# Kernel optimization log

Measured on AMD Instinct MI355X. Metric: run time of the kernel, lower is better.

Reference implementation:

```python
import jax, jax.numpy as jnp
import numpy as np

# dims: H hops, N nodes, F = nfeat, HID = hidden, C = nclass
H, N, F, HID, C = 10, 100000, 256, 512, 47
ALPHA = 0.5  # GCNII alpha in FeedForwardNetII


def setup_inputs() -> dict:
    key = jax.random.key(0)
    ks = jax.random.split(key, 16)
    s = lambda i, shape, scale: jax.random.normal(ks[i], shape, jnp.float32) * scale
    return {
        "features": s(0, (H, N, F), 1.0),        # stacked feature_list
        "label_emb": s(1, (N, C), 1.0),
        # lr_att: Linear(2F, 1)
        "wa": s(2, (2 * F,), 0.05),
        "ba": jnp.zeros((), jnp.float32),
        # lr_output = FeedForwardNetII(F, HID, C, n_layers_2=4, alpha)
        "w0": s(3, (F, HID), 0.05), "b0": jnp.zeros((HID,), jnp.float32),
        "wg1": s(4, (HID, HID), 0.04),
        "wg2": s(5, (HID, HID), 0.04),
        "w_last": s(6, (HID, C), 0.05), "b_last": jnp.zeros((C,), jnp.float32),
        "a_out": jnp.full((), 0.25, jnp.float32),  # PReLU slope
        # label_fc = FeedForwardNet(C, HID, C, n_layers_3=4)
        "wl0": s(7, (C, HID), 0.1), "bl0": jnp.zeros((HID,), jnp.float32),
        "wl1": s(8, (HID, HID), 0.04), "bl1": jnp.zeros((HID,), jnp.float32),
        "wl2": s(9, (HID, HID), 0.04), "bl2": jnp.zeros((HID,), jnp.float32),
        "wl3": s(10, (HID, C), 0.05), "bl3": jnp.zeros((C,), jnp.float32),
        "a_lab": jnp.full((), 0.25, jnp.float32),
    }


def _prelu(x, a):
    return jnp.where(x >= 0, x, a * x)


def _act(x):  # act = leaky_relu(0.2)
    return jax.nn.leaky_relu(x, 0.2)


def reference(features, label_emb, wa, ba, w0, b0, wg1, wg2, w_last, b_last, a_out,
              wl0, bl0, wl1, bl1, wl2, bl2, wl3, bl3, a_lab):
    # lr_att(cat([a, b])) == a @ wl + b @ wr + ba
    wl, wr = wa[:F], wa[F:]
    xr = jnp.einsum('hnf,f->hn', features, wr)  # right-half projection of each hop
    # hop 0: cat([X0, X0])
    scores = [_act(features[0] @ wl + xr[0] + ba)]  # list of [N]
    for i in range(1, H):
        att = jax.nn.softmax(jnp.stack(scores, axis=1), axis=1)       # [N, i]
        history = jnp.einsum('hnf,nh->nf', features[:i], att)          # [N, F]
        scores.append(_act(history @ wl + xr[i] + ba))
    att = jax.nn.softmax(jnp.stack(scores, axis=1), axis=1)            # [N, H]
    right = jnp.einsum('hnf,nh->nf', features, att)                    # [N, F]

    x = right @ w0 + b0
    h0 = x
    for wg in (wg1, wg2):
        xi = _prelu(x, a_out)
        support = (1.0 - ALPHA) * xi + ALPHA * h0
        x = support @ wg + xi  # GraphConvolution adds its input back
    x = _prelu(x, a_out) @ w_last + b_last                             # [N, C]

    # label_fc: FeedForwardNet, 4 linear layers with PReLU between
    y = _prelu(label_emb @ wl0 + bl0, a_lab)
    y = _prelu(y @ wl1 + bl1, a_lab)
    y = _prelu(y @ wl2 + bl2, a_lab)
    y = y @ wl3 + bl3                                                  # [N, C]
    return x + y
```

## Files before the change

### kernel.cpp

```cpp
#include <hip/hip_runtime.h>
#include <cstdint>
#include <cstddef>


#define DEVI __device__ __forceinline__

typedef __attribute__((ext_vector_type(4))) float fx4;
typedef __attribute__((ext_vector_type(8))) short sx8;

constexpr int NN = 100000;

DEVI unsigned short f2b(float f) {
  unsigned u = __float_as_uint(f);
  u = (u + 0x7fffu + ((u >> 16) & 1u)) >> 16;
  return (unsigned short)u;
}
DEVI float b2f(short v) {
  return __uint_as_float(((unsigned)(unsigned short)v) << 16);
}

#define GLDS16(gp, lp) __builtin_amdgcn_global_load_lds( \
    (__attribute__((address_space(1))) void*)(void*)(gp), \
    (__attribute__((address_space(3))) void*)(lp), 16, 0, 0)

__global__ __launch_bounds__(256)
void attn_kernel(const float* __restrict__ feat, const float* __restrict__ wa,
                 const float* __restrict__ baP, short* __restrict__ right) {
  const int lane = threadIdx.x & 63;
  const int n = blockIdx.x * 4 + (threadIdx.x >> 6);
  const float ba = *baP;
  const fx4 wl4 = *(const fx4*)(wa + lane * 4);
  const fx4 wr4 = *(const fx4*)(wa + 256 + lane * 4);
  fx4 f[10];
  float xl[10], xr[10];
#pragma unroll
  for (int h = 0; h < 10; h++) {
    f[h] = *(const fx4*)(feat + ((long)h * NN + n) * 256 + lane * 4);
    float pl = f[h][0] * wl4[0] + f[h][1] * wl4[1] + f[h][2] * wl4[2] + f[h][3] * wl4[3];
    float pr = f[h][0] * wr4[0] + f[h][1] * wr4[1] + f[h][2] * wr4[2] + f[h][3] * wr4[3];
#pragma unroll
    for (int off = 32; off > 0; off >>= 1) {
      pl += __shfl_xor(pl, off);
      pr += __shfl_xor(pr, off);
    }
    xl[h] = pl; xr[h] = pr;
  }
  float e[10];
  float s = xl[0] + xr[0] + ba;
  s = s >= 0.f ? s : 0.2f * s;
  e[0] = __expf(s);
  float P = e[0] * xl[0], S = e[0];
#pragma unroll
  for (int i = 1; i < 10; i++) {
    float t = P / S + xr[i] + ba;
    t = t >= 0.f ? t : 0.2f * t;
    e[i] = __expf(t);
    P += e[i] * xl[i];
    S += e[i];
  }
  const float inv = 1.f / S;
  fx4 r = {0.f, 0.f, 0.f, 0.f};
#pragma unroll
  for (int h = 0; h < 10; h++) {
    const float w = e[h] * inv;
    r[0] += w * f[h][0]; r[1] += w * f[h][1];
    r[2] += w * f[h][2]; r[3] += w * f[h][3];
  }
  ushort4 o;
  o.x = f2b(r[0]); o.y = f2b(r[1]); o.z = f2b(r[2]); o.w = f2b(r[3]);
  *(ushort4*)(right + (long)n * 256 + lane * 4) = o;
}

__global__ void pack_wt(const float* __restrict__ src, short* __restrict__ dst,
                        int Ksrc, int Nsrc, int padK, int padN) {
  int idx = blockIdx.x * 256 + threadIdx.x;
  if (idx >= padK * padN) return;
  int n = idx / padK, k = idx - n * padK;
  float v = (k < Ksrc && n < Nsrc) ? src[(long)k * Nsrc + n] : 0.f;
  dst[idx] = (short)f2b(v);
}

__global__ void pack_lab(const float* __restrict__ src, short* __restrict__ dst) {
  long idx = (long)blockIdx.x * 256 + threadIdx.x;
  if (idx >= (long)NN * 64) return;
  int n = (int)(idx >> 6), k = (int)(idx & 63);
  dst[idx] = (short)f2b(k < 47 ? src[(long)n * 47 + k] : 0.f);
}

template<int BN, int EPI>
__global__ __launch_bounds__(256)
void gemm_bt(const short* __restrict__ A, const short* __restrict__ BT, const int K,
             const float* __restrict__ bias, const short* __restrict__ epiIn,
             short* __restrict__ out0, short* __restrict__ out1,
             const float* __restrict__ alphaP, const float* __restrict__ xout,
             float* __restrict__ fout) {
  constexpr int BM = 128, BK = 32;
  constexpr int WN = BN / 2;
  constexpr int FM = 4, FN = WN / 16;
  __shared__ short As[BM * BK];
  __shared__ short Bs[BN * BK];
  const int tid = threadIdx.x;
  const int wave = tid >> 6, lane = tid & 63;
  const int wm = wave >> 1, wn = wave & 1;
  const int m0 = blockIdx.x * BM;
  const int n0 = blockIdx.y * BN;
  fx4 acc[FM][FN] = {};

  const int kIters = K / BK;
  for (int kk = 0; kk < kIters; kk++) {
    const int k0 = kk * BK;
#pragma unroll
    for (int c = 0; c < (BM * BK) / (256 * 8); c++) {
      const int idx = c * 256 + tid;
      long row = m0 + (idx >> 2);
      if (row > NN - 1) row = NN - 1;
      const short* gp = A + row * (long)K + k0 + ((idx & 3) << 3);
      GLDS16(gp, As + idx * 8);
    }
#pragma unroll
    for (int c = 0; c < (BN * BK) / (256 * 8); c++) {
      const int idx = c * 256 + tid;
      const short* gp = BT + (long)(n0 + (idx >> 2)) * K + k0 + ((idx & 3) << 3);
      GLDS16(gp, Bs + idx * 8);
    }
    __syncthreads();
    sx8 af[FM], bf[FN];
#pragma unroll
    for (int i = 0; i < FM; i++)
      af[i] = *(const sx8*)(As + (wm * 64 + i * 16 + (lane & 15)) * BK + ((lane >> 4) << 3));
#pragma unroll
    for (int j = 0; j < FN; j++)
      bf[j] = *(const sx8*)(Bs + (wn * WN + j * 16 + (lane & 15)) * BK + ((lane >> 4) << 3));
#pragma unroll
    for (int i = 0; i < FM; i++)
#pragma unroll
      for (int j = 0; j < FN; j++)
        acc[i][j] = __builtin_amdgcn_mfma_f32_16x16x32_bf16(af[i], bf[j], acc[i][j], 0, 0, 0);
    __syncthreads();
  }

  const float alpha = (alphaP != nullptr) ? *alphaP : 0.f;
#pragma unroll
  for (int i = 0; i < FM; i++) {
#pragma unroll
    for (int j = 0; j < FN; j++) {
#pragma unroll
      for (int r = 0; r < 4; r++) {
        const int m = m0 + wm * 64 + i * 16 + ((lane >> 4) << 2) + r;
        const int n = n0 + wn * WN + j * 16 + (lane & 15);
        if (m >= NN) continue;
        float v = acc[i][j][r];
        const long o = (long)m * 512 + n;
        if constexpr (EPI == 0) {
          v += bias[n];
          out0[o] = (short)f2b(v);
          const float p = v >= 0.f ? v : alpha * v;
          out1[o] = (short)f2b(0.5f * p + 0.5f * v);
        } else if constexpr (EPI == 1) {
          const float x0v = b2f(epiIn[o]);
          const float xi = x0v >= 0.f ? x0v : alpha * x0v;
          const float x1 = v + xi;
          out0[o] = (short)f2b(x1);
          const float p1 = x1 >= 0.f ? x1 : alpha * x1;
          out1[o] = (short)f2b(0.5f * p1 + 0.5f * x0v);
        } else if constexpr (EPI == 2) {
          const float x1v = b2f(epiIn[o]);
          const float xi = x1v >= 0.f ? x1v : alpha * x1v;
          const float x2 = v + xi;
          out0[o] = (short)f2b(x2 >= 0.f ? x2 : alpha * x2);
        } else if constexpr (EPI == 3) {
          const float bv = (n < 47) ? bias[n] : 0.f;
          fout[(long)m * 64 + n] = v + bv;
        } else if constexpr (EPI == 4) {
          const float y = v + bias[n];
          out0[o] = (short)f2b(y >= 0.f ? y : alpha * y);
        } else {
          if (n < 47) fout[(long)m * 47 + n] = v + bias[n] + xout[(long)m * 64 + n];
        }
      }
    }
  }
}

constexpr long  OFF_W0T  = 0;
constexpr long  OFF_WG1T = 131072;
constexpr long  OFF_WG2T = 393216;
constexpr long  OFF_WLST = 655360;
constexpr long  OFF_WL0T = 688128;
constexpr long  OFF_WL1T = 720896;
constexpr long  OFF_WL2T = 983040;
constexpr long  OFF_WL3T = 1245184;
constexpr size_t B_RIGHT = 2560000;
constexpr size_t B_LAB   = 53760000;
constexpr size_t B_XOUT  = 66560000;
constexpr size_t B_B1    = 92160000;
constexpr size_t B_B2    = 194560000;
constexpr size_t B_B3    = 296960000;
constexpr size_t B_B4    = 399360000;
constexpr size_t WS_NEED = 501760000;

extern "C" void kernel_launch(void* const* d_in, const int* in_sizes, int n_in,
                              void* d_out, int out_size, void* d_ws, size_t ws_size,
                              hipStream_t stream) {
  const float* features  = (const float*)d_in[0];
  const float* label_emb = (const float*)d_in[1];
  const float* wa     = (const float*)d_in[2];
  const float* ba     = (const float*)d_in[3];
  const float* w0     = (const float*)d_in[4];
  const float* b0     = (const float*)d_in[5];
  const float* wg1    = (const float*)d_in[6];
  const float* wg2    = (const float*)d_in[7];
  const float* w_last = (const float*)d_in[8];
  const float* b_last = (const float*)d_in[9];
  const float* a_out  = (const float*)d_in[10];
  const float* wl0    = (const float*)d_in[11];
  const float* bl0    = (const float*)d_in[12];
  const float* wl1    = (const float*)d_in[13];
  const float* bl1    = (const float*)d_in[14];
  const float* wl2    = (const float*)d_in[15];
  const float* bl2    = (const float*)d_in[16];
  const float* wl3    = (const float*)d_in[17];
  const float* bl3    = (const float*)d_in[18];
  const float* a_lab  = (const float*)d_in[19];

  if (ws_size < WS_NEED) return;

  char*  ws    = (char*)d_ws;
  short* WP    = (short*)ws;
  short* right = (short*)(ws + B_RIGHT);
  short* lab   = (short*)(ws + B_LAB);
  float* xoutb = (float*)(ws + B_XOUT);
  short* B1    = (short*)(ws + B_B1);
  short* B2    = (short*)(ws + B_B2);
  short* B3    = (short*)(ws + B_B3);
  short* B4    = (short*)(ws + B_B4);

  auto pk = [&](const float* s, long off, int Ks, int Ns, int pK, int pN) {
    int tot = pK * pN;
    pack_wt<<<dim3((tot + 255) / 256), dim3(256), 0, stream>>>(s, WP + off, Ks, Ns, pK, pN);
  };
  pk(w0,     OFF_W0T,  256, 512, 256, 512);
  pk(wg1,    OFF_WG1T, 512, 512, 512, 512);
  pk(wg2,    OFF_WG2T, 512, 512, 512, 512);
  pk(w_last, OFF_WLST, 512, 47,  512, 64);
  pk(wl0,    OFF_WL0T, 47,  512, 64,  512);
  pk(wl1,    OFF_WL1T, 512, 512, 512, 512);
  pk(wl2,    OFF_WL2T, 512, 512, 512, 512);
  pk(wl3,    OFF_WL3T, 512, 47,  512, 64);
  pack_lab<<<dim3(25000), dim3(256), 0, stream>>>(label_emb, lab);

  attn_kernel<<<dim3(25000), dim3(256), 0, stream>>>(features, wa, ba, right);

  const dim3 blk(256);
  const dim3 g512(782, 4), g64(782, 1);
  gemm_bt<128, 0><<<g512, blk, 0, stream>>>(right, WP + OFF_W0T, 256, b0, nullptr,
                                            B1, B2, a_out, nullptr, nullptr);
  gemm_bt<128, 1><<<g512, blk, 0, stream>>>(B2, WP + OFF_WG1T, 512, nullptr, B1,
                                            B3, B4, a_out, nullptr, nullptr);
  gemm_bt<128, 2><<<g512, blk, 0, stream>>>(B4, WP + OFF_WG2T, 512, nullptr, B3,
                                            B1, nullptr, a_out, nullptr, nullptr);
  gemm_bt<64, 3><<<g64, blk, 0, stream>>>(B1, WP + OFF_WLST, 512, b_last, nullptr,
                                          nullptr, nullptr, nullptr, nullptr, xoutb);
  gemm_bt<128, 4><<<g512, blk, 0, stream>>>(lab, WP + OFF_WL0T, 64, bl0, nullptr,
                                            B2, nullptr, a_lab, nullptr, nullptr);
  gemm_bt<128, 4><<<g512, blk, 0, stream>>>(B2, WP + OFF_WL1T, 512, bl1, nullptr,
                                            B3, nullptr, a_lab, nullptr, nullptr);
  gemm_bt<128, 4><<<g512, blk, 0, stream>>>(B3, WP + OFF_WL2T, 512, bl2, nullptr,
                                            B4, nullptr, a_lab, nullptr, nullptr);
  gemm_bt<64, 5><<<g64, blk, 0, stream>>>(B4, WP + OFF_WL3T, 512, bl3, nullptr,
                                          nullptr, nullptr, nullptr, xoutb, (float*)d_out);
}
```

Measured before the change: 2.350 ms.

## Pair branch GEMMs per launch, fuse final projections, merge packing kernels

Replaces the nine packing kernels with a single packing kernel. The GCNII branch and the label_fc branch now run side by side, one layer of each per dual-GEMM launch, so each launch fills more of the GPU. The two output projections (w_last and wl3) are concatenated along K into one GEMM that writes the final sum directly. This removes the fp32 xout intermediate and several launches, at the cost of a larger workspace; when the workspace is too small, a sequential fallback path is used.

```diff
diff --git a/kernel.cpp b/kernel.cpp
--- a/kernel.cpp
+++ b/kernel.cpp
@@ -71,133 +71,222 @@
   *(ushort4*)(right + (long)n * 256 + lane * 4) = o;
 }
 
-__global__ void pack_wt(const float* __restrict__ src, short* __restrict__ dst,
-                        int Ksrc, int Nsrc, int padK, int padN) {
-  int idx = blockIdx.x * 256 + threadIdx.x;
-  if (idx >= padK * padN) return;
-  int n = idx / padK, k = idx - n * padK;
-  float v = (k < Ksrc && n < Nsrc) ? src[(long)k * Nsrc + n] : 0.f;
-  dst[idx] = (short)f2b(v);
-}
-
-__global__ void pack_lab(const float* __restrict__ src, short* __restrict__ dst) {
-  long idx = (long)blockIdx.x * 256 + threadIdx.x;
-  if (idx >= (long)NN * 64) return;
-  int n = (int)(idx >> 6), k = (int)(idx & 63);
-  dst[idx] = (short)f2b(k < 47 ? src[(long)n * 47 + k] : 0.f);
-}
-
-template<int BN, int EPI>
+constexpr int W_W0  = 0;
+constexpr int W_WG1 = 131072;
+constexpr int W_WG2 = 393216;
+constexpr int W_WL0 = 655360;
+constexpr int W_WL1 = 688128;
+constexpr int W_WL2 = 950272;
+constexpr int W_FIN = 1212416;
+constexpr int W_END = 1277952;
+
 __global__ __launch_bounds__(256)
-void gemm_bt(const short* __restrict__ A, const short* __restrict__ BT, const int K,
-             const float* __restrict__ bias, const short* __restrict__ epiIn,
-             short* __restrict__ out0, short* __restrict__ out1,
-             const float* __restrict__ alphaP, const float* __restrict__ xout,
-             float* __restrict__ fout) {
-  constexpr int BM = 128, BK = 32;
-  constexpr int WN = BN / 2;
-  constexpr int FM = 4, FN = WN / 16;
+void uber_pack(const float* __restrict__ w0,     const float* __restrict__ wg1,
+               const float* __restrict__ wg2,    const float* __restrict__ wl0,
+               const float* __restrict__ wl1,    const float* __restrict__ wl2,
+               const float* __restrict__ w_last, const float* __restrict__ wl3,
+               const float* __restrict__ lemb,
+               short* __restrict__ WP, short* __restrict__ lab) {
+  const long idx = (long)blockIdx.x * 256 + threadIdx.x;
+  constexpr long LAB_END = (long)W_END + (long)NN * 64;
+  if (idx >= LAB_END) return;
+  if (idx < W_WG1) {
+    int l = (int)idx, n = l >> 8, k = l & 255;
+    WP[idx] = (short)f2b(w0[(long)k * 512 + n]);
+  } else if (idx < W_WG2) {
+    int l = (int)(idx - W_WG1), n = l >> 9, k = l & 511;
+    WP[idx] = (short)f2b(wg1[(long)k * 512 + n]);
+  } else if (idx < W_WL0) {
+    int l = (int)(idx - W_WG2), n = l >> 9, k = l & 511;
+    WP[idx] = (short)f2b(wg2[(long)k * 512 + n]);
+  } else if (idx < W_WL1) {
+    int l = (int)(idx - W_WL0), n = l >> 6, k = l & 63;
+    WP[idx] = (short)f2b(k < 47 ? wl0[(long)k * 512 + n] : 0.f);
+  } else if (idx < W_WL2) {
+    int l = (int)(idx - W_WL1), n = l >> 9, k = l & 511;
+    WP[idx] = (short)f2b(wl1[(long)k * 512 + n]);
+  } else if (idx < W_FIN) {
+    int l = (int)(idx - W_WL2), n = l >> 9, k = l & 511;
+    WP[idx] = (short)f2b(wl2[(long)k * 512 + n]);
+  } else if (idx < W_FIN + 32768) {
+    int l = (int)(idx - W_FIN), n = l >> 9, k = l & 511;
+    WP[W_FIN + (long)n * 1024 + k] = (short)f2b(n < 47 ? w_last[(long)k * 47 + n] : 0.f);
+  } else if (idx < W_END) {
+    int l = (int)(idx - (W_FIN + 32768)), n = l >> 9, k = l & 511;
+    WP[W_FIN + (long)n * 1024 + 512 + k] = (short)f2b(n < 47 ? wl3[(long)k * 47 + n] : 0.f);
+  } else {
+    long l = idx - W_END;
+    int n = (int)(l >> 6), k = (int)(l & 63);
+    lab[l] = (short)f2b(k < 47 ? lemb[(long)n * 47 + k] : 0.f);
+  }
+}
+
+struct GArgs {
+  const short* A; const short* BT; int K;
+  const float* bias; const short* epiIn;
+  short* out0; short* out1; const float* alphaP;
+};
+
+template<int EPI>
+DEVI void epilogue(const GArgs& g, const fx4 (&acc)[4][4],
+                   int m0, int n0, int wm, int wn, int lane) {
+  const float alpha = (g.alphaP != nullptr) ? *g.alphaP : 0.f;
+#pragma unroll
+  for (int i = 0; i < 4; i++) {
+#pragma unroll
+    for (int j = 0; j < 4; j++) {
+#pragma unroll
+      for (int r = 0; r < 4; r++) {
+        const int m = m0 + wm * 64 + i * 16 + ((lane >> 4) << 2) + r;
+        const int n = n0 + wn * 64 + j * 16 + (lane & 15);
+        if (m >= NN) continue;
+        float v = acc[i][j][r];
+        const long o = (long)m * 512 + n;
+        if constexpr (EPI == 0) {
+          v += g.bias[n];
+          g.out0[o] = (short)f2b(v);
+          const float p = v >= 0.f ? v : alpha * v;
+          g.out1[o] = (short)f2b(0.5f * p + 0.5f * v);
+        } else if constexpr (EPI == 1) {
+          const float x0v = b2f(g.epiIn[o]);
+          const float xi = x0v >= 0.f ? x0v : alpha * x0v;
+          const float x1 = v + xi;
+          g.out0[o] = (short)f2b(x1);
+          const float p1 = x1 >= 0.f ? x1 : alpha * x1;
+          g.out1[o] = (short)f2b(0.5f * p1 + 0.5f * x0v);
+        } else if constexpr (EPI == 2) {
+          const float x1v = b2f(g.epiIn[o]);
+          const float xi = x1v >= 0.f ? x1v : alpha * x1v;
+          const float x2 = v + xi;
+          g.out0[o] = (short)f2b(x2 >= 0.f ? x2 : alpha * x2);
+        } else {
+          const float y = v + g.bias[n];
+          g.out0[o] = (short)f2b(y >= 0.f ? y : alpha * y);
+        }
+      }
+    }
+  }
+}
+
+template<int EA, int EB>
+__global__ __launch_bounds__(256)
+void gemm_dual(GArgs ga, GArgs gb) {
+  constexpr int BM = 128, BN = 128, BK = 32;
+  __shared__ short As[BM * BK];
+  __shared__ short Bs[BN * BK];
+  const bool second = (blockIdx.y >= 4);
+  const short* __restrict__ A  = second ? gb.A  : ga.A;
+  const short* __restrict__ BT = second ? gb.BT : ga.BT;
+  const int K = second ? gb.K : ga.K;
+  const int tid = threadIdx.x;
+  const int wave = tid >> 6, lane = tid & 63;
+  const int wm = wave >> 1, wn = wave & 1;
+  const int m0 = blockIdx.x * BM;
+  const int n0 = (blockIdx.y & 3) * BN;
+  fx4 acc[4][4] = {};
+
+  const int kIters = K / BK;
+  for (int kk = 0; kk < kIters; kk++) {
+    const int k0 = kk * BK;
+#pragma unroll
+    for (int c = 0; c < 2; c++) {
+      const int idx = c * 256 + tid;
+      long row = m0 + (idx >> 2);
+      if (row > NN - 1) row = NN - 1;
+      GLDS16(A + row * (long)K + k0 + ((idx & 3) << 3), As + idx * 8);
+    }
+#pragma unroll
+    for (int c = 0; c < 2; c++) {
+      const int idx = c * 256 + tid;
+      GLDS16(BT + (long)(n0 + (idx >> 2)) * K + k0 + ((idx & 3) << 3), Bs + idx * 8);
+    }
+    __syncthreads();
+    sx8 af[4], bf[4];
+#pragma unroll
+    for (int i = 0; i < 4; i++)
+      af[i] = *(const sx8*)(As + (wm * 64 + i * 16 + (lane & 15)) * BK + ((lane >> 4) << 3));
+#pragma unroll
+    for (int j = 0; j < 4; j++)
+      bf[j] = *(const sx8*)(Bs + (wn * 64 + j * 16 + (lane & 15)) * BK + ((lane >> 4) << 3));
+#pragma unroll
+    for (int i = 0; i < 4; i++)
+#pragma unroll
+      for (int j = 0; j < 4; j++)
+        acc[i][j] = __builtin_amdgcn_mfma_f32_16x16x32_bf16(af[i], bf[j], acc[i][j], 0, 0, 0);
+    __syncthreads();
+  }
+
+  if (!second) epilogue<EA>(ga, acc, m0, n0, wm, wn, lane);
+  else         epilogue<EB>(gb, acc, m0, n0, wm, wn, lane);
+}
+
+__global__ __launch_bounds__(256)
+void gemm_final(const short* __restrict__ Ap, const short* __restrict__ Ay,
+                const short* __restrict__ BT, const float* __restrict__ b1,
+                const float* __restrict__ b2, float* __restrict__ outp) {
+  constexpr int BM = 128, BN = 64, BK = 32, WN = 32;
   __shared__ short As[BM * BK];
   __shared__ short Bs[BN * BK];
   const int tid = threadIdx.x;
   const int wave = tid >> 6, lane = tid & 63;
   const int wm = wave >> 1, wn = wave & 1;
   const int m0 = blockIdx.x * BM;
-  const int n0 = blockIdx.y * BN;
-  fx4 acc[FM][FN] = {};
-
-  const int kIters = K / BK;
-  for (int kk = 0; kk < kIters; kk++) {
+  fx4 acc[4][2] = {};
+
+  for (int kk = 0; kk < 32; kk++) {
     const int k0 = kk * BK;
-#pragma unroll
-    for (int c = 0; c < (BM * BK) / (256 * 8); c++) {
+    const short* __restrict__ Asel = (kk < 16) ? Ap : Ay;
+    const int kl = k0 & 511;
+#pragma unroll
+    for (int c = 0; c < 2; c++) {
       const int idx = c * 256 + tid;
       long row = m0 + (idx >> 2);
       if (row > NN - 1) row = NN - 1;
-      const short* gp = A + row * (long)K + k0 + ((idx & 3) << 3);
-      GLDS16(gp, As + idx * 8);
-    }
-#pragma unroll
-    for (int c = 0; c < (BN * BK) / (256 * 8); c++) {
-      const int idx = c * 256 + tid;
-      const short* gp = BT + (long)(n0 + (idx >> 2)) * K + k0 + ((idx & 3) << 3);
-      GLDS16(gp, Bs + idx * 8);
+      GLDS16(Asel + row * 512L + kl + ((idx & 3) << 3), As + idx * 8);
+    }
+    {
+      const int idx = tid;
+      GLDS16(BT + (long)(idx >> 2) * 1024 + k0 + ((idx & 3) << 3), Bs + idx * 8);
     }
     __syncthreads();
-    sx8 af[FM], bf[FN];
-#pragma unroll
-    for (int i = 0; i < FM; i++)
+    sx8 af[4], bf[2];
+#pragma unroll
+    for (int i = 0; i < 4; i++)
       af[i] = *(const sx8*)(As + (wm * 64 + i * 16 + (lane & 15)) * BK + ((lane >> 4) << 3));
 #pragma unroll
-    for (int j = 0; j < FN; j++)
+    for (int j = 0; j < 2; j++)
       bf[j] = *(const sx8*)(Bs + (wn * WN + j * 16 + (lane & 15)) * BK + ((lane >> 4) << 3));
 #pragma unroll
-    for (int i = 0; i < FM; i++)
-#pragma unroll
-      for (int j = 0; j < FN; j++)
+    for (int i = 0; i < 4; i++)
+#pragma unroll
+      for (int j = 0; j < 2; j++)
         acc[i][j] = __builtin_amdgcn_mfma_f32_16x16x32_bf16(af[i], bf[j], acc[i][j], 0, 0, 0);
     __syncthreads();
   }
 
-  const float alpha = (alphaP != nullptr) ? *alphaP : 0.f;
-#pragma unroll
-  for (int i = 0; i < FM; i++) {
-#pragma unroll
-    for (int j = 0; j < FN; j++) {
+#pragma unroll
+  for (int i = 0; i < 4; i++)
+#pragma unroll
+    for (int j = 0; j < 2; j++)
 #pragma unroll
       for (int r = 0; r < 4; r++) {
         const int m = m0 + wm * 64 + i * 16 + ((lane >> 4) << 2) + r;
-        const int n = n0 + wn * WN + j * 16 + (lane & 15);
-        if (m >= NN) continue;
-        float v = acc[i][j][r];
-        const long o = (long)m * 512 + n;
-        if constexpr (EPI == 0) {
-          v += bias[n];
-          out0[o] = (short)f2b(v);
-          const float p = v >= 0.f ? v : alpha * v;
-          out1[o] = (short)f2b(0.5f * p + 0.5f * v);
-        } else if constexpr (EPI == 1) {
-          const float x0v = b2f(epiIn[o]);
-          const float xi = x0v >= 0.f ? x0v : alpha * x0v;
-          const float x1 = v + xi;
-          out0[o] = (short)f2b(x1);
-          const float p1 = x1 >= 0.f ? x1 : alpha * x1;
-          out1[o] = (short)f2b(0.5f * p1 + 0.5f * x0v);
-        } else if constexpr (EPI == 2) {
-          const float x1v = b2f(epiIn[o]);
-          const float xi = x1v >= 0.f ? x1v : alpha * x1v;
-          const float x2 = v + xi;
-          out0[o] = (short)f2b(x2 >= 0.f ? x2 : alpha * x2);
-        } else if constexpr (EPI == 3) {
-          const float bv = (n < 47) ? bias[n] : 0.f;
-          fout[(long)m * 64 + n] = v + bv;
-        } else if constexpr (EPI == 4) {
-          const float y = v + bias[n];
-          out0[o] = (short)f2b(y >= 0.f ? y : alpha * y);
-        } else {
-          if (n < 47) fout[(long)m * 47 + n] = v + bias[n] + xout[(long)m * 64 + n];
-        }
+        const int n = wn * WN + j * 16 + (lane & 15);
+        if (m < NN && n < 47)
+          outp[(long)m * 47 + n] = acc[i][j][r] + b1[n] + b2[n];
       }
-    }
-  }
-}
-
-constexpr long  OFF_W0T  = 0;
-constexpr long  OFF_WG1T = 131072;
-constexpr long  OFF_WG2T = 393216;
-constexpr long  OFF_WLST = 655360;
-constexpr long  OFF_WL0T = 688128;
-constexpr long  OFF_WL1T = 720896;
-constexpr long  OFF_WL2T = 983040;
-constexpr long  OFF_WL3T = 1245184;
+}
+
 constexpr size_t B_RIGHT = 2560000;
 constexpr size_t B_LAB   = 53760000;
-constexpr size_t B_XOUT  = 66560000;
-constexpr size_t B_B1    = 92160000;
-constexpr size_t B_B2    = 194560000;
-constexpr size_t B_B3    = 296960000;
-constexpr size_t B_B4    = 399360000;
-constexpr size_t WS_NEED = 501760000;
+constexpr size_t B_B1    = 66560000;
+constexpr size_t B_B2    = 168960000;
+constexpr size_t B_B3    = 271360000;
+constexpr size_t B_B4    = 373760000;
+constexpr size_t B_B5    = 476160000;
+constexpr size_t B_B6    = 578560000;
+constexpr size_t WS_PRIMARY  = 680960000;
+constexpr size_t WS_FALLBACK = 476160000;
 
 extern "C" void kernel_launch(void* const* d_in, const int* in_sizes, int n_in,
                               void* d_out, int out_size, void* d_ws, size_t ws_size,
@@ -223,50 +312,53 @@
   const float* bl3    = (const float*)d_in[18];
   const float* a_lab  = (const float*)d_in[19];
 
-  if (ws_size < WS_NEED) return;
+  if (ws_size < WS_FALLBACK) return;
 
   char*  ws    = (char*)d_ws;
   short* WP    = (short*)ws;
   short* right = (short*)(ws + B_RIGHT);
   short* lab   = (short*)(ws + B_LAB);
-  float* xoutb = (float*)(ws + B_XOUT);
-  short* B1    = (short*)(ws + B_B1);
-  short* B2    = (short*)(ws + B_B2);
-  short* B3    = (short*)(ws + B_B3);
-  short* B4    = (short*)(ws + B_B4);
-
-  auto pk = [&](const float* s, long off, int Ks, int Ns, int pK, int pN) {
-    int tot = pK * pN;
-    pack_wt<<<dim3((tot + 255) / 256), dim3(256), 0, stream>>>(s, WP + off, Ks, Ns, pK, pN);
-  };
-  pk(w0,     OFF_W0T,  256, 512, 256, 512);
-  pk(wg1,    OFF_WG1T, 512, 512, 512, 512);
-  pk(wg2,    OFF_WG2T, 512, 512, 512, 512);
-  pk(w_last, OFF_WLST, 512, 47,  512, 64);
-  pk(wl0,    OFF_WL0T, 47,  512, 64,  512);
-  pk(wl1,    OFF_WL1T, 512, 512, 512, 512);
-  pk(wl2,    OFF_WL2T, 512, 512, 512, 512);
-  pk(wl3,    OFF_WL3T, 512, 47,  512, 64);
-  pack_lab<<<dim3(25000), dim3(256), 0, stream>>>(label_emb, lab);
+  short* C1    = (short*)(ws + B_B1);
+  short* C2    = (short*)(ws + B_B2);
+  short* C3    = (short*)(ws + B_B3);
+  short* C4    = (short*)(ws + B_B4);
+
+  uber_pack<<<dim3(29992), dim3(256), 0, stream>>>(
+      w0, wg1, wg2, wl0, wl1, wl2, w_last, wl3, label_emb, WP, lab);
 
   attn_kernel<<<dim3(25000), dim3(256), 0, stream>>>(features, wa, ba, right);
 
   const dim3 blk(256);
-  const dim3 g512(782, 4), g64(782, 1);
-  gemm_bt<128, 0><<<g512, blk, 0, stream>>>(right, WP + OFF_W0T, 256, b0, nullptr,
-                                            B1, B2, a_out, nullptr, nullptr);
-  gemm_bt<128, 1><<<g512, blk, 0, stream>>>(B2, WP + OFF_WG1T, 512, nullptr, B1,
-                                            B3, B4, a_out, nullptr, nullptr);
-  gemm_bt<128, 2><<<g512, blk, 0, stream>>>(B4, WP + OFF_WG2T, 512, nullptr, B3,
-                                            B1, nullptr, a_out, nullptr, nullptr);
-  gemm_bt<64, 3><<<g64, blk, 0, stream>>>(B1, WP + OFF_WLST, 512, b_last, nullptr,
-                                          nullptr, nullptr, nullptr, nullptr, xoutb);
-  gemm_bt<128, 4><<<g512, blk, 0, stream>>>(lab, WP + OFF_WL0T, 64, bl0, nullptr,
-                                            B2, nullptr, a_lab, nullptr, nullptr);
-  gemm_bt<128, 4><<<g512, blk, 0, stream>>>(B2, WP + OFF_WL1T, 512, bl1, nullptr,
-                                            B3, nullptr, a_lab, nullptr, nullptr);
-  gemm_bt<128, 4><<<g512, blk, 0, stream>>>(B3, WP + OFF_WL2T, 512, bl2, nullptr,
-                                            B4, nullptr, a_lab, nullptr, nullptr);
-  gemm_bt<64, 5><<<g64, blk, 0, stream>>>(B4, WP + OFF_WL3T, 512, bl3, nullptr,
-                                          nullptr, nullptr, nullptr, xoutb, (float*)d_out);
-}
+  const dim3 gDual(782, 8), gSingle(782, 4), gFin(782, 1);
+
+  if (ws_size >= WS_PRIMARY) {
+    short* C5 = (short*)(ws + B_B5);
+    short* C6 = (short*)(ws + B_B6);
+    GArgs a0{right, WP + W_W0,  256, b0,  nullptr, C1, C2,      a_out};
+    GArgs l0{lab,   WP + W_WL0,  64, bl0, nullptr, C5, nullptr, a_lab};
+    gemm_dual<0, 4><<<gDual, blk, 0, stream>>>(a0, l0);
+    GArgs a1{C2, WP + W_WG1, 512, nullptr, C1, C3, C4,      a_out};
+    GArgs l1{C5, WP + W_WL1, 512, bl1,    nullptr, C6, nullptr, a_lab};
+    gemm_dual<1, 4><<<gDual, blk, 0, stream>>>(a1, l1);
+    GArgs a2{C4, WP + W_WG2, 512, nullptr, C3, C1, nullptr, a_out};
+    GArgs l2{C6, WP + W_WL2, 512, bl2,    nullptr, C2, nullptr, a_lab};
+    gemm_dual<2, 4><<<gDual, blk, 0, stream>>>(a2, l2);
+    gemm_final<<<gFin, blk, 0, stream>>>(C1, C2, WP + W_FIN, b_last, bl3,
+                                         (float*)d_out);
+  } else {
+    GArgs a0{right, WP + W_W0,  256, b0,      nullptr, C1, C2,      a_out};
+    gemm_dual<0, 0><<<gSingle, blk, 0, stream>>>(a0, a0);
+    GArgs a1{C2,    WP + W_WG1, 512, nullptr, C1,      C3, C4,      a_out};
+    gemm_dual<1, 1><<<gSingle, blk, 0, stream>>>(a1, a1);
+    GArgs a2{C4,    WP + W_WG2, 512, nullptr, C3,      C2, nullptr, a_out};
+    gemm_dual<2, 2><<<gSingle, blk, 0, stream>>>(a2, a2);
+    GArgs l0{lab, WP + W_WL0,  64, bl0, nullptr, C1, nullptr, a_lab};
+    gemm_dual<4, 4><<<gSingle, blk, 0, stream>>>(l0, l0);
+    GArgs l1{C1,  WP + W_WL1, 512, bl1, nullptr, C3, nullptr, a_lab};
+    gemm_dual<4, 4><<<gSingle, blk, 0, stream>>>(l1, l1);
+    GArgs l2{C3,  WP + W_WL2, 512, bl2, nullptr, C1, nullptr, a_lab};
+    gemm_dual<4, 4><<<gSingle, blk, 0, stream>>>(l2, l2);
+    gemm_final<<<gFin, blk, 0, stream>>>(C2, C1, WP + W_FIN, b_last, bl3,
+                                         (float*)d_out);
+  }
+}
```

Result: faster. 2.276 ms (-3.2%).
